# Optimization experiments

Measured on AMD Instinct MI355X. Metric: run time of the kernel, lower is better.

The kernel has to match this reference:

```python
import jax, jax.numpy as jnp
import numpy as np

DIM = 192
BASE = 10000.0
DIM_X = DIM // 3
DIM_Y = DIM // 3
DIM_T = DIM - 2 * (DIM // 3)


def _inv_freq(d):
    return 1.0 / (BASE ** (jnp.arange(0, d, 2, dtype=jnp.float32) / d))


def setup_inputs() -> dict:
    key = jax.random.key(0)
    frames, height, width = 32, 64, 64
    x = jax.random.normal(key, (1, frames * height * width, DIM), dtype=jnp.float32)
    return {"x": x, "height": height, "width": width, "frames": frames}


def reference(x, height, width, frames):
    dtype = x.dtype
    # per-axis angle tables: [len, dim_axis/2] -> duplicated to [len, dim_axis]
    fx = jnp.arange(width, dtype=jnp.float32)[:, None] * _inv_freq(DIM_X)[None, :]
    fy = jnp.arange(height, dtype=jnp.float32)[:, None] * _inv_freq(DIM_Y)[None, :]
    ft = jnp.arange(frames, dtype=jnp.float32)[:, None] * _inv_freq(DIM_T)[None, :]
    fx = jnp.concatenate([fx, fx], axis=-1)  # [W, DIM_X]
    fy = jnp.concatenate([fy, fy], axis=-1)  # [H, DIM_Y]
    ft = jnp.concatenate([ft, ft], axis=-1)  # [T, DIM_T]

    def grid(ax, ay, at):
        # broadcast each axis table over the (T, H, W) grid, concat on feature dim
        gx = jnp.broadcast_to(ax[None, None, :, :], (frames, height, width, DIM_X))
        gy = jnp.broadcast_to(ay[None, :, None, :], (frames, height, width, DIM_Y))
        gt = jnp.broadcast_to(at[:, None, None, :], (frames, height, width, DIM_T))
        return jnp.concatenate([gx, gy, gt], axis=-1).reshape(frames * height * width, DIM)

    cos_3d = grid(jnp.cos(fx), jnp.cos(fy), jnp.cos(ft)).astype(dtype)
    sin_3d = grid(jnp.sin(fx), jnp.sin(fy), jnp.sin(ft)).astype(dtype)
    return (cos_3d, sin_3d)
```

## Files before the change

### kernel.cpp

```cpp
#include <hip/hip_runtime.h>


#define NPOS (32 * 64 * 64)
#define DIM 192

#define NEG_C (-0.41524101186092027f)
#define LOG2_INV_2PI (-2.6514961294723187f)
#define R1 0.7498942093324559f
#define R2 0.5623413251903491f
#define R3 0.4216965034285822f

typedef float f32x4 __attribute__((ext_vector_type(4)));

__global__ __launch_bounds__(256) void rope3d_kernel(float* __restrict__ out) {
    const unsigned int i = blockIdx.x * 256u + threadIdx.x;
    const unsigned int r = i / 48u;
    const unsigned int c = i - r * 48u;

    const unsigned int t = r >> 12;
    const unsigned int h = (r >> 6) & 63u;
    const unsigned int w = r & 63u;

    const unsigned int axis = c >> 4;
    const float pos = (float)(axis == 0 ? w : (axis == 1 ? h : t));

    const unsigned int inner0 = (c * 4u) & 31u;
    const float fr0 = __builtin_exp2f(fmaf((float)inner0, NEG_C, LOG2_INV_2PI));
    const float fr1 = fr0 * R1;
    const float fr2 = fr0 * R2;
    const float fr3 = fr0 * R3;

    const float a0 = __builtin_amdgcn_fractf(pos * fr0);
    const float a1 = __builtin_amdgcn_fractf(pos * fr1);
    const float a2 = __builtin_amdgcn_fractf(pos * fr2);
    const float a3 = __builtin_amdgcn_fractf(pos * fr3);

    const f32x4 cv = { __builtin_amdgcn_cosf(a0), __builtin_amdgcn_cosf(a1),
                       __builtin_amdgcn_cosf(a2), __builtin_amdgcn_cosf(a3) };
    const f32x4 sv = { __builtin_amdgcn_sinf(a0), __builtin_amdgcn_sinf(a1),
                       __builtin_amdgcn_sinf(a2), __builtin_amdgcn_sinf(a3) };

    const size_t base = (size_t)i * 4u;
    __builtin_nontemporal_store(cv, (f32x4*)(out + base));
    __builtin_nontemporal_store(sv, (f32x4*)(out + (size_t)NPOS * DIM + base));
}

extern "C" void kernel_launch(void* const* d_in, const int* in_sizes, int n_in,
                              void* d_out, int out_size, void* d_ws, size_t ws_size,
                              hipStream_t stream) {
    (void)d_in; (void)in_sizes; (void)n_in; (void)d_ws; (void)ws_size; (void)out_size;
    float* out = (float*)d_out;
    const unsigned int total4 = NPOS * 48u;
    const unsigned int blocks = total4 / 256u;
    rope3d_kernel<<<blocks, 256, 0, stream>>>(out);
}
```

Baseline: 244.1 us.

## Split cos and sin outputs across alternating waves, doubling thread count

Result: no change. 243.2 us (-0.4%).

```diff
diff --git a/kernel.cpp b/kernel.cpp
--- a/kernel.cpp
+++ b/kernel.cpp
@@ -3,6 +3,7 @@
 
 #define NPOS (32 * 64 * 64)
 #define DIM 192
+#define TOTAL4 (NPOS * 48u)
 
 #define NEG_C (-0.41524101186092027f)
 #define LOG2_INV_2PI (-2.6514961294723187f)
@@ -10,10 +11,13 @@
 #define R2 0.5623413251903491f
 #define R3 0.4216965034285822f
 
-typedef float f32x4 __attribute__((ext_vector_type(4)));
+__global__ __launch_bounds__(256) void rope3d_kernel(float* __restrict__ out) {
+    const unsigned int tid = blockIdx.x * 256u + threadIdx.x;
+    const unsigned int wave = tid >> 6;
+    const unsigned int lane = tid & 63u;
+    const unsigned int is_sin = wave & 1u;
+    const unsigned int i = (wave >> 1) * 64u + lane;
 
-__global__ __launch_bounds__(256) void rope3d_kernel(float* __restrict__ out) {
-    const unsigned int i = blockIdx.x * 256u + threadIdx.x;
     const unsigned int r = i / 48u;
     const unsigned int c = i - r * 48u;
 
@@ -35,14 +39,21 @@
     const float a2 = __builtin_amdgcn_fractf(pos * fr2);
     const float a3 = __builtin_amdgcn_fractf(pos * fr3);
 
-    const f32x4 cv = { __builtin_amdgcn_cosf(a0), __builtin_amdgcn_cosf(a1),
-                       __builtin_amdgcn_cosf(a2), __builtin_amdgcn_cosf(a3) };
-    const f32x4 sv = { __builtin_amdgcn_sinf(a0), __builtin_amdgcn_sinf(a1),
-                       __builtin_amdgcn_sinf(a2), __builtin_amdgcn_sinf(a3) };
+    float v0, v1, v2, v3;
+    if (is_sin) {
+        v0 = __builtin_amdgcn_sinf(a0);
+        v1 = __builtin_amdgcn_sinf(a1);
+        v2 = __builtin_amdgcn_sinf(a2);
+        v3 = __builtin_amdgcn_sinf(a3);
+    } else {
+        v0 = __builtin_amdgcn_cosf(a0);
+        v1 = __builtin_amdgcn_cosf(a1);
+        v2 = __builtin_amdgcn_cosf(a2);
+        v3 = __builtin_amdgcn_cosf(a3);
+    }
 
-    const size_t base = (size_t)i * 4u;
-    __builtin_nontemporal_store(cv, (f32x4*)(out + base));
-    __builtin_nontemporal_store(sv, (f32x4*)(out + (size_t)NPOS * DIM + base));
+    const size_t base = (size_t)is_sin * ((size_t)NPOS * DIM) + (size_t)i * 4u;
+    *(float4*)(out + base) = make_float4(v0, v1, v2, v3);
 }
 
 extern "C" void kernel_launch(void* const* d_in, const int* in_sizes, int n_in,
@@ -50,7 +61,7 @@
                               hipStream_t stream) {
     (void)d_in; (void)in_sizes; (void)n_in; (void)d_ws; (void)ws_size; (void)out_size;
     float* out = (float*)d_out;
-    const unsigned int total4 = NPOS * 48u;
-    const unsigned int blocks = total4 / 256u;
+    const unsigned int total_threads = TOTAL4 * 2u;
+    const unsigned int blocks = total_threads / 256u;
     rope3d_kernel<<<blocks, 256, 0, stream>>>(out);
 }
```
